# Optimization experiments

Hardware: AMD Instinct MI355X
Metric: run time of the kernel (lower is better)

The kernel has to match this reference:

```python
import jax, jax.numpy as jnp
import numpy as np

WS = 7       # window size
SHIFT = 3    # shift size (ws//2)
NH = 16      # num heads
DIM = 512    # channels
HH = 112
WW = 112
HIDDEN = int(DIM * 4.0)
EPS = 1e-5


def _rel_index():
    # Swin relative position index, [N, N] ints into the bias table
    coords = np.stack(np.meshgrid(np.arange(WS), np.arange(WS), indexing='ij')).reshape(2, -1)
    rel = coords[:, :, None] - coords[:, None, :]
    rel = rel.transpose(1, 2, 0) + (WS - 1)
    rel[:, :, 0] *= 2 * WS - 1
    return rel.sum(-1)


def _attn_mask():
    # shifted-window mask on HH x WW (already multiples of WS) -> [nW, N, N] with 0 / -1e9
    img = np.zeros((HH, WW), np.int32)
    cnt = 0
    sl = (slice(0, -WS), slice(-WS, -SHIFT), slice(-SHIFT, None))
    for h in sl:
        for w in sl:
            img[h, w] = cnt
            cnt += 1
    win = img.reshape(HH // WS, WS, WW // WS, WS).transpose(0, 2, 1, 3).reshape(-1, WS * WS)
    diff = win[:, None, :] - win[:, :, None]
    return np.where(diff == 0, 0.0, -1e9).astype(np.float32)


def setup_inputs() -> dict:
    key = jax.random.key(0)
    ks = jax.random.split(key, 8)
    s = 0.02
    return {
        'x': jax.random.normal(ks[0], (DIM, HH, WW), jnp.float32),
        'norm1_w': jnp.ones((DIM,), jnp.float32),
        'norm1_b': jnp.zeros((DIM,), jnp.float32),
        'qkv_w': jax.random.normal(ks[1], (3 * DIM, DIM), jnp.float32) * s,
        'qkv_b': jnp.zeros((3 * DIM,), jnp.float32),
        'proj_w': jax.random.normal(ks[2], (DIM, DIM), jnp.float32) * s,
        'proj_b': jnp.zeros((DIM,), jnp.float32),
        'rpb_table': jax.random.normal(ks[3], ((2 * WS - 1) ** 2, NH), jnp.float32) * s,
        'norm2_w': jnp.ones((DIM,), jnp.float32),
        'norm2_b': jnp.zeros((DIM,), jnp.float32),
        'fc1_w': jax.random.normal(ks[4], (HIDDEN, DIM), jnp.float32) * s,
        'fc1_b': jnp.zeros((HIDDEN,), jnp.float32),
        'fc2_w': jax.random.normal(ks[5], (DIM, HIDDEN), jnp.float32) * s,
        'fc2_b': jnp.zeros((DIM,), jnp.float32),
    }


def _ln(x_hwc, w, b):
    m = x_hwc.mean(-1, keepdims=True)
    v = x_hwc.var(-1, keepdims=True)
    return (x_hwc - m) / jnp.sqrt(v + EPS) * w + b


def reference(x, norm1_w, norm1_b, qkv_w, qkv_b, proj_w, proj_b, rpb_table,
              norm2_w, norm2_b, fc1_w, fc1_b, fc2_w, fc2_b):
    C, H, W = x.shape
    ws = WS
    N = ws * ws
    hd = C // NH
    scale = 1.0 / np.sqrt(hd).astype(np.float32)

    x_hwc = jnp.moveaxis(x, 0, -1)                       # [H,W,C]
    xn = _ln(x_hwc, norm1_w, norm1_b)
    xs = jnp.roll(xn, (-SHIFT, -SHIFT), (0, 1))          # cyclic shift
    # window partition -> [nW, N, C]
    xw = xs.reshape(H // ws, ws, W // ws, ws, C).transpose(0, 2, 1, 3, 4).reshape(-1, N, C)

    qkv = xw @ qkv_w.T + qkv_b                            # [nW,N,3C]
    q, k, v = jnp.split(qkv, 3, -1)
    heads = lambda t: t.reshape(-1, N, NH, hd).transpose(0, 2, 1, 3)  # [nW,H,N,hd]
    q, k, v = heads(q), heads(k), heads(v)

    attn = jnp.einsum('whnd,whmd->whnm', q * scale, k)    # [nW,H,N,N]
    idx = jnp.asarray(_rel_index().reshape(-1))
    bias = rpb_table[idx].reshape(N, N, NH).transpose(2, 0, 1)  # [H,N,N]
    mask = jnp.asarray(_attn_mask())                       # [nW,N,N]
    attn = attn + bias[None] + mask[:, None]
    attn = jax.nn.softmax(attn, -1)

    out = jnp.einsum('whnm,whmd->whnd', attn, v).transpose(0, 2, 1, 3).reshape(-1, N, C)
    out = out @ proj_w.T + proj_b
    # window unpartition + reverse shift
    out = out.reshape(H // ws, W // ws, ws, ws, C).transpose(0, 2, 1, 3, 4).reshape(H, W, C)
    out = jnp.roll(out, (SHIFT, SHIFT), (0, 1))

    x1 = x_hwc + out                                       # residual (DropPath rate 0)
    x2 = _ln(x1, norm2_w, norm2_b)
    h = jax.nn.gelu(x2.reshape(-1, C) @ fc1_w.T + fc1_b)
    m = (h @ fc2_w.T + fc2_b).reshape(H, W, C)
    y = x1 + m
    return jnp.moveaxis(y, -1, 0)                          # back to [C,H,W]
```

## Files before the change

### kernel.cpp

```cpp
#include <hip/hip_runtime.h>

#define NPIX 12544
#define CDIM 512
#define QKVN 1536
#define HIDDEN 2048

typedef unsigned short u16;
typedef unsigned int u32;

typedef short bf16x8 __attribute__((ext_vector_type(8)));
typedef float f32x4 __attribute__((ext_vector_type(4)));

static __device__ __forceinline__ u16 f2bf(float f) {
  u32 u = __float_as_uint(f);
  return (u16)((u + 0x7fffu + ((u >> 16) & 1u)) >> 16);
}
static __device__ __forceinline__ float bf2f(u32 bits16) {
  return __uint_as_float(bits16 << 16);
}
static __device__ __forceinline__ u32 pack2(float a, float b) {
  return (u32)f2bf(a) | ((u32)f2bf(b) << 16);
}
static __device__ __forceinline__ void unpack8(uint4 u, float* d) {
  d[0] = bf2f(u.x & 0xffffu); d[1] = bf2f(u.x >> 16);
  d[2] = bf2f(u.y & 0xffffu); d[3] = bf2f(u.y >> 16);
  d[4] = bf2f(u.z & 0xffffu); d[5] = bf2f(u.z >> 16);
  d[6] = bf2f(u.w & 0xffffu); d[7] = bf2f(u.w >> 16);
}
static __device__ __forceinline__ void async_ld16(const void* g, void* l) {
  __builtin_amdgcn_global_load_lds((__attribute__((address_space(1))) void*)g,
                                   (__attribute__((address_space(3))) void*)l, 16, 0, 0);
}

__global__ __launch_bounds__(256) void f32_to_bf16(const float* __restrict__ in, u16* __restrict__ out) {
  const int i = blockIdx.x * 256 + threadIdx.x;
  const float4 v = ((const float4*)in)[i];
  ushort4 u;
  u.x = f2bf(v.x); u.y = f2bf(v.y); u.z = f2bf(v.z); u.w = f2bf(v.w);
  ((ushort4*)out)[i] = u;
}

__global__ __launch_bounds__(256) void ln1_partial(const float* __restrict__ x,
                                                   float* __restrict__ psum, float* __restrict__ pssq) {
  const int p = blockIdx.x * 256 + threadIdx.x;
  const int c0 = blockIdx.y * 32;
  float s = 0.f, ss = 0.f;
#pragma unroll
  for (int c = 0; c < 32; c++) {
    const float v = x[(long)(c0 + c) * NPIX + p];
    s += v; ss += v * v;
  }
  psum[blockIdx.y * NPIX + p] = s;
  pssq[blockIdx.y * NPIX + p] = ss;
}

__global__ __launch_bounds__(256) void ln1_stats(const float* __restrict__ psum, const float* __restrict__ pssq,
                                                 float* __restrict__ mean, float* __restrict__ rstd) {
  const int p = blockIdx.x * 256 + threadIdx.x;
  float s = 0.f, ss = 0.f;
#pragma unroll
  for (int ch = 0; ch < 16; ch++) { s += psum[ch * NPIX + p]; ss += pssq[ch * NPIX + p]; }
  const float m = s * (1.f / 512.f);
  const float v = ss * (1.f / 512.f) - m * m;
  mean[p] = m;
  rstd[p] = rsqrtf(v + 1e-5f);
}

__global__ __launch_bounds__(256) void ln1_shift_part(const float* __restrict__ x,
    const float* __restrict__ mean, const float* __restrict__ rstd,
    const float* __restrict__ gw, const float* __restrict__ gb, u16* __restrict__ xw) {
  __shared__ float tile[32][65];
  const int p0 = blockIdx.x * 64;
  const int c0 = blockIdx.y * 32;
  const int t = threadIdx.x;
  {
    const int pl = t & 63;
    const int cl0 = t >> 6;
#pragma unroll
    for (int r = 0; r < 8; r++) {
      const int cl = r * 4 + cl0;
      tile[cl][pl] = x[(long)(c0 + cl) * NPIX + p0 + pl];
    }
  }
  __syncthreads();
  const int cl = t & 31;
  const int g = t >> 5;
  const float wc = gw[c0 + cl];
  const float bc = gb[c0 + cl];
#pragma unroll
  for (int pass = 0; pass < 8; pass++) {
    const int pl = pass * 8 + g;
    const int p = p0 + pl;
    const int h = p / 112;
    const int w = p - h * 112;
    int hs = h + 109; if (hs >= 112) hs -= 112;
    int ws2 = w + 109; if (ws2 >= 112) ws2 -= 112;
    const int hq = hs / 7, wq = ws2 / 7;
    const int tok = (hq * 16 + wq) * 49 + (hs - hq * 7) * 7 + (ws2 - wq * 7);
    const float val = (tile[cl][pl] - mean[p]) * rstd[p] * wc + bc;
    xw[(long)tok * 512 + c0 + cl] = f2bf(val);
  }
}

template<bool OUT_BF16, bool DO_GELU, bool REMAP>
__global__ __launch_bounds__(256, 2) void gemm_bt(
    const u16* __restrict__ A, const u16* __restrict__ B,
    const float* __restrict__ bias, void* __restrict__ out,
    const int N, const int K) {
  __shared__ __align__(16) u16 Asm[128 * 32];
  __shared__ __align__(16) u16 Bsm[128 * 32];
  const int M0 = blockIdx.x << 7;
  const int N0 = blockIdx.y << 7;
  const int t = threadIdx.x;
  const int wave = t >> 6;
  const int lane = t & 63;
  const int l15 = lane & 15;
  const int quad = lane >> 4;
  const int wm = wave & 1;
  const int wn = wave >> 1;

  f32x4 acc[4][4] = {};

  for (int k0 = 0; k0 < K; k0 += 32) {
#pragma unroll
    for (int i = 0; i < 2; i++) {
      const int flatbase = i * 256 + wave * 64;
      const int FL = flatbase + lane;
      const int row = FL >> 2;
      const int chunk = FL & 3;
      async_ld16(A + (long)(M0 + row) * K + k0 + chunk * 8, &Asm[flatbase * 8]);
      async_ld16(B + (long)(N0 + row) * K + k0 + chunk * 8, &Bsm[flatbase * 8]);
    }
    __syncthreads();
    bf16x8 af[4], bfr[4];
#pragma unroll
    for (int im = 0; im < 4; im++)
      af[im] = *(const bf16x8*)&Asm[(wm * 64 + im * 16 + l15) * 32 + quad * 8];
#pragma unroll
    for (int in = 0; in < 4; in++)
      bfr[in] = *(const bf16x8*)&Bsm[(wn * 64 + in * 16 + l15) * 32 + quad * 8];
#pragma unroll
    for (int im = 0; im < 4; im++)
#pragma unroll
      for (int in = 0; in < 4; in++)
        acc[im][in] = __builtin_amdgcn_mfma_f32_16x16x32_bf16(af[im], bfr[in], acc[im][in], 0, 0, 0);
    __syncthreads();
  }

#pragma unroll
  for (int im = 0; im < 4; im++) {
#pragma unroll
    for (int in = 0; in < 4; in++) {
      const int col = N0 + wn * 64 + in * 16 + l15;
      const float bv = bias[col];
#pragma unroll
      for (int r = 0; r < 4; r++) {
        const int row = M0 + wm * 64 + im * 16 + quad * 4 + r;
        float v = acc[im][in][r] + bv;
        if (DO_GELU) {
          const float z2 = 1.5957691216f * (v + 0.044715f * v * v * v);
          v = v / (1.0f + __expf(-z2));
        }
        long orow = row;
        if (REMAP) {
          const int win = row / 49;
          const int nn = row - win * 49;
          const int nq = nn / 7;
          const int hs = (win >> 4) * 7 + nq;
          const int wsx = (win & 15) * 7 + (nn - nq * 7);
          int h = hs + 3; if (h >= 112) h -= 112;
          int w = wsx + 3; if (w >= 112) w -= 112;
          orow = h * 112 + w;
        }
        if (OUT_BF16) ((u16*)out)[orow * (long)N + col] = f2bf(v);
        else          ((float*)out)[orow * (long)N + col] = v;
      }
    }
  }
}

__global__ __launch_bounds__(64) void attn_kernel(
    const u16* __restrict__ qkv, const float* __restrict__ rpb, u16* __restrict__ out) {
  const int win = blockIdx.x >> 4;
  const int head = blockIdx.x & 15;
  __shared__ __align__(16) float ks[49][32];
  __shared__ __align__(16) float vs[49][32];
  __shared__ float bias_s[169];
  __shared__ int label_s[49];
  const int l = threadIdx.x;
  for (int idx = l; idx < 169; idx += 64) bias_s[idx] = rpb[idx * 16 + head];
  float q[32];
  if (l < 49) {
    const long base = (long)(win * 49 + l) * 1536 + head * 32;
    const uint4* qp = (const uint4*)(qkv + base);
    const uint4* kp = (const uint4*)(qkv + base + 512);
    const uint4* vp = (const uint4*)(qkv + base + 1024);
#pragma unroll
    for (int cc = 0; cc < 4; cc++) {
      unpack8(qp[cc], &q[cc * 8]);
      unpack8(kp[cc], &ks[l][cc * 8]);
      unpack8(vp[cc], &vs[l][cc * 8]);
    }
    const int ri = l / 7, ci = l - (l / 7) * 7;
    const int hs = (win >> 4) * 7 + ri;
    const int wsx = (win & 15) * 7 + ci;
    label_s[l] = (hs < 105 ? 0 : (hs < 109 ? 1 : 2)) * 3 + (wsx < 105 ? 0 : (wsx < 109 ? 1 : 2));
  }
  __syncthreads();
  if (l >= 49) return;
  const int ri = l / 7, ci = l - (l / 7) * 7;
  const int mylab = label_s[l];
  float sr[49];
  float mx = -1e30f;
#pragma unroll
  for (int j = 0; j < 49; j++) {
    const float4* kj = (const float4*)ks[j];
    float s = 0.f;
#pragma unroll
    for (int c = 0; c < 8; c++) {
      const float4 kv = kj[c];
      s += q[c * 4 + 0] * kv.x + q[c * 4 + 1] * kv.y + q[c * 4 + 2] * kv.z + q[c * 4 + 3] * kv.w;
    }
    const int rj = j / 7, cj = j - (j / 7) * 7;
    float sv = s * 0.17677669529663687f + bias_s[(ri - rj + 6) * 13 + (ci - cj + 6)];
    if (mylab != label_s[j]) sv -= 1e9f;
    sr[j] = sv;
    mx = fmaxf(mx, sv);
  }
  float sum = 0.f;
#pragma unroll
  for (int j = 0; j < 49; j++) { const float e = __expf(sr[j] - mx); sr[j] = e; sum += e; }
  float o[32];
#pragma unroll
  for (int d = 0; d < 32; d++) o[d] = 0.f;
#pragma unroll
  for (int j = 0; j < 49; j++) {
    const float pj = sr[j];
    const float4* vj = (const float4*)vs[j];
#pragma unroll
    for (int c = 0; c < 8; c++) {
      const float4 vv = vj[c];
      o[c * 4 + 0] += pj * vv.x; o[c * 4 + 1] += pj * vv.y;
      o[c * 4 + 2] += pj * vv.z; o[c * 4 + 3] += pj * vv.w;
    }
  }
  const float inv = 1.f / sum;
  uint4* outp = (uint4*)(out + (long)(win * 49 + l) * 512 + head * 32);
#pragma unroll
  for (int cc = 0; cc < 4; cc++) {
    uint4 u;
    u.x = pack2(o[cc * 8 + 0] * inv, o[cc * 8 + 1] * inv);
    u.y = pack2(o[cc * 8 + 2] * inv, o[cc * 8 + 3] * inv);
    u.z = pack2(o[cc * 8 + 4] * inv, o[cc * 8 + 5] * inv);
    u.w = pack2(o[cc * 8 + 6] * inv, o[cc * 8 + 7] * inv);
    outp[cc] = u;
  }
}

__global__ __launch_bounds__(256) void resid_kernel(const float* __restrict__ x,
    const float* __restrict__ proj, float* __restrict__ x1) {
  __shared__ float tile[32][65];
  const int p0 = blockIdx.x * 64;
  const int c0 = blockIdx.y * 32;
  const int t = threadIdx.x;
  {
    const int pl = t & 63;
    const int cl0 = t >> 6;
#pragma unroll
    for (int r = 0; r < 8; r++) {
      const int cl = r * 4 + cl0;
      tile[cl][pl] = x[(long)(c0 + cl) * NPIX + p0 + pl];
    }
  }
  __syncthreads();
  const int cl = t & 31;
  const int g = t >> 5;
#pragma unroll
  for (int pass = 0; pass < 8; pass++) {
    const int pl = pass * 8 + g;
    const long idx = (long)(p0 + pl) * 512 + c0 + cl;
    x1[idx] = tile[cl][pl] + proj[idx];
  }
}

__global__ __launch_bounds__(256) void ln2_apply(const float* __restrict__ x1,
    const float* __restrict__ gw, const float* __restrict__ gb, u16* __restrict__ x2) {
  const int wave = threadIdx.x >> 6;
  const int lane = threadIdx.x & 63;
  const int p = blockIdx.x * 4 + wave;
  const float4* row = (const float4*)(x1 + (long)p * 512);
  const float4 a = row[lane * 2];
  const float4 b = row[lane * 2 + 1];
  float s = a.x + a.y + a.z + a.w + b.x + b.y + b.z + b.w;
  float ss = a.x * a.x + a.y * a.y + a.z * a.z + a.w * a.w
           + b.x * b.x + b.y * b.y + b.z * b.z + b.w * b.w;
#pragma unroll
  for (int o = 32; o > 0; o >>= 1) { s += __shfl_xor(s, o); ss += __shfl_xor(ss, o); }
  const float m = s * (1.f / 512.f);
  const float var = ss * (1.f / 512.f) - m * m;
  const float rs = rsqrtf(var + 1e-5f);
  const float4 w0 = ((const float4*)gw)[lane * 2];
  const float4 w1 = ((const float4*)gw)[lane * 2 + 1];
  const float4 b0 = ((const float4*)gb)[lane * 2];
  const float4 b1 = ((const float4*)gb)[lane * 2 + 1];
  uint4 u;
  u.x = pack2((a.x - m) * rs * w0.x + b0.x, (a.y - m) * rs * w0.y + b0.y);
  u.y = pack2((a.z - m) * rs * w0.z + b0.z, (a.w - m) * rs * w0.w + b0.w);
  u.z = pack2((b.x - m) * rs * w1.x + b1.x, (b.y - m) * rs * w1.y + b1.y);
  u.w = pack2((b.z - m) * rs * w1.z + b1.z, (b.w - m) * rs * w1.w + b1.w);
  ((uint4*)(x2 + (long)p * 512))[lane] = u;
}

__global__ __launch_bounds__(256) void final_kernel(const float* __restrict__ x1,
    const float* __restrict__ mm, float* __restrict__ y) {
  __shared__ float tile[32][65];
  const int p0 = blockIdx.x * 64;
  const int c0 = blockIdx.y * 32;
  const int t = threadIdx.x;
  {
    const int cl = t & 31;
    const int g = t >> 5;
#pragma unroll
    for (int pass = 0; pass < 8; pass++) {
      const int pl = pass * 8 + g;
      const long idx = (long)(p0 + pl) * 512 + c0 + cl;
      tile[cl][pl] = x1[idx] + mm[idx];
    }
  }
  __syncthreads();
  const int pl = t & 63;
  const int cl0 = t >> 6;
#pragma unroll
  for (int r = 0; r < 8; r++) {
    const int cl = r * 4 + cl0;
    y[(long)(c0 + cl) * NPIX + p0 + pl] = tile[cl][pl];
  }
}

extern "C" void kernel_launch(void* const* d_in, const int* in_sizes, int n_in,
                              void* d_out, int out_size, void* d_ws, size_t ws_size,
                              hipStream_t stream) {
  (void)in_sizes; (void)n_in; (void)out_size; (void)ws_size;
  const float* x      = (const float*)d_in[0];
  const float* n1w    = (const float*)d_in[1];
  const float* n1b    = (const float*)d_in[2];
  const float* qkv_w  = (const float*)d_in[3];
  const float* qkv_b  = (const float*)d_in[4];
  const float* proj_w = (const float*)d_in[5];
  const float* proj_b = (const float*)d_in[6];
  const float* rpb    = (const float*)d_in[7];
  const float* n2w    = (const float*)d_in[8];
  const float* n2b    = (const float*)d_in[9];
  const float* fc1_w  = (const float*)d_in[10];
  const float* fc1_b  = (const float*)d_in[11];
  const float* fc2_w  = (const float*)d_in[12];
  const float* fc2_b  = (const float*)d_in[13];
  float* y = (float*)d_out;

  char* base = (char*)d_ws;
  size_t off = 0;
  auto alloc = [&](size_t b) { char* p = base + off; off += (b + 255) & ~(size_t)255; return p; };
  float* mean1 = (float*)alloc((size_t)NPIX * 4);
  float* rstd1 = (float*)alloc((size_t)NPIX * 4);
  float* psum  = (float*)alloc((size_t)16 * NPIX * 4);
  float* pssq  = (float*)alloc((size_t)16 * NPIX * 4);
  u16* Wq = (u16*)alloc((size_t)QKVN * CDIM * 2);
  u16* Wp = (u16*)alloc((size_t)CDIM * CDIM * 2);
  u16* W1 = (u16*)alloc((size_t)HIDDEN * CDIM * 2);
  u16* W2 = (u16*)alloc((size_t)CDIM * HIDDEN * 2);
  u16* bufA = (u16*)alloc((size_t)NPIX * CDIM * 2);
  char* bufB = alloc((size_t)NPIX * QKVN * 2);
  float* x1 = (float*)alloc((size_t)NPIX * CDIM * 4);
  u16* hbuf = (u16*)alloc((size_t)NPIX * HIDDEN * 2);

  u16* xw      = bufA;
  u16* qkvbuf  = (u16*)bufB;
  u16* attnout = bufA;
  float* projout = (float*)bufB;
  u16* x2 = bufA;
  float* mbuf = (float*)bufB;

  f32_to_bf16<<<QKVN * CDIM / 1024, 256, 0, stream>>>(qkv_w, Wq);
  f32_to_bf16<<<CDIM * CDIM / 1024, 256, 0, stream>>>(proj_w, Wp);
  f32_to_bf16<<<HIDDEN * CDIM / 1024, 256, 0, stream>>>(fc1_w, W1);
  f32_to_bf16<<<CDIM * HIDDEN / 1024, 256, 0, stream>>>(fc2_w, W2);

  ln1_partial<<<dim3(49, 16), 256, 0, stream>>>(x, psum, pssq);
  ln1_stats<<<49, 256, 0, stream>>>(psum, pssq, mean1, rstd1);
  ln1_shift_part<<<dim3(196, 16), 256, 0, stream>>>(x, mean1, rstd1, n1w, n1b, xw);

  gemm_bt<true, false, false><<<dim3(98, QKVN / 128), 256, 0, stream>>>(xw, Wq, qkv_b, qkvbuf, QKVN, CDIM);
  attn_kernel<<<256 * 16, 64, 0, stream>>>(qkvbuf, rpb, attnout);
  gemm_bt<false, false, true><<<dim3(98, CDIM / 128), 256, 0, stream>>>(attnout, Wp, proj_b, projout, CDIM, CDIM);

  resid_kernel<<<dim3(196, 16), 256, 0, stream>>>(x, projout, x1);
  ln2_apply<<<NPIX / 4, 256, 0, stream>>>(x1, n2w, n2b, x2);

  gemm_bt<true, true, false><<<dim3(98, HIDDEN / 128), 256, 0, stream>>>(x2, W1, fc1_b, hbuf, HIDDEN, CDIM);
  gemm_bt<false, false, false><<<dim3(98, CDIM / 128), 256, 0, stream>>>(hbuf, W2, fc2_b, mbuf, CDIM, HIDDEN);

  final_kernel<<<dim3(196, 16), 256, 0, stream>>>(x1, mbuf, y);
}
```

Measured before the change: 382.0 us.

## Rewrite window attention with bf16 MFMA and a precomputed bias-mask table

Replaces the scalar per-thread window attention (one 64-thread block per window-head, with fp32 dot products in registers) with an MFMA kernel. Each wave handles one head of a window, with QK^T and PV done via 16x16x32 bf16 MFMA, swizzled LDS layouts for V-transpose and P, and softmax reductions done with cross-lane shuffles. A new prepass builds a padded 64x64 bias-plus-mask table per (window class, head), so the attention kernel does a single load per score instead of index math and label comparisons. The change also rounds P and the outputs by bf16 truncation rather than round-to-nearest, which adds some precision risk.

```diff
diff --git a/kernel.cpp b/kernel.cpp
--- a/kernel.cpp
+++ b/kernel.cpp
@@ -15,17 +15,11 @@
   u32 u = __float_as_uint(f);
   return (u16)((u + 0x7fffu + ((u >> 16) & 1u)) >> 16);
 }
-static __device__ __forceinline__ float bf2f(u32 bits16) {
-  return __uint_as_float(bits16 << 16);
-}
 static __device__ __forceinline__ u32 pack2(float a, float b) {
   return (u32)f2bf(a) | ((u32)f2bf(b) << 16);
 }
-static __device__ __forceinline__ void unpack8(uint4 u, float* d) {
-  d[0] = bf2f(u.x & 0xffffu); d[1] = bf2f(u.x >> 16);
-  d[2] = bf2f(u.y & 0xffffu); d[3] = bf2f(u.y >> 16);
-  d[4] = bf2f(u.z & 0xffffu); d[5] = bf2f(u.z >> 16);
-  d[6] = bf2f(u.w & 0xffffu); d[7] = bf2f(u.w >> 16);
+static __device__ __forceinline__ u32 packtrunc2(float lo, float hi) {
+  return __builtin_amdgcn_perm(__float_as_uint(hi), __float_as_uint(lo), 0x07060302u);
 }
 static __device__ __forceinline__ void async_ld16(const void* g, void* l) {
   __builtin_amdgcn_global_load_lds((__attribute__((address_space(1))) void*)g,
@@ -179,81 +173,164 @@
   }
 }
 
-__global__ __launch_bounds__(64) void attn_kernel(
-    const u16* __restrict__ qkv, const float* __restrict__ rpb, u16* __restrict__ out) {
-  const int win = blockIdx.x >> 4;
+__global__ __launch_bounds__(256) void build_biasT(const float* __restrict__ rpb, float* __restrict__ biasT) {
+  const int cls = blockIdx.x >> 4;
   const int head = blockIdx.x & 15;
-  __shared__ __align__(16) float ks[49][32];
-  __shared__ __align__(16) float vs[49][32];
-  __shared__ float bias_s[169];
-  __shared__ int label_s[49];
-  const int l = threadIdx.x;
-  for (int idx = l; idx < 169; idx += 64) bias_s[idx] = rpb[idx * 16 + head];
-  float q[32];
-  if (l < 49) {
-    const long base = (long)(win * 49 + l) * 1536 + head * 32;
-    const uint4* qp = (const uint4*)(qkv + base);
-    const uint4* kp = (const uint4*)(qkv + base + 512);
-    const uint4* vp = (const uint4*)(qkv + base + 1024);
-#pragma unroll
-    for (int cc = 0; cc < 4; cc++) {
-      unpack8(qp[cc], &q[cc * 8]);
-      unpack8(kp[cc], &ks[l][cc * 8]);
-      unpack8(vp[cc], &vs[l][cc * 8]);
-    }
-    const int ri = l / 7, ci = l - (l / 7) * 7;
-    const int hs = (win >> 4) * 7 + ri;
-    const int wsx = (win & 15) * 7 + ci;
-    label_s[l] = (hs < 105 ? 0 : (hs < 109 ? 1 : 2)) * 3 + (wsx < 105 ? 0 : (wsx < 109 ? 1 : 2));
+  for (int e = threadIdx.x; e < 4096; e += 256) {
+    const int j = e >> 6;
+    const int i = e & 63;
+    float v;
+    if (j >= 49) v = -1e9f;
+    else if (i >= 49) v = 0.f;
+    else {
+      const int ri = i / 7, ci = i - (i / 7) * 7;
+      const int rj = j / 7, cj = j - (j / 7) * 7;
+      v = rpb[((ri - rj + 6) * 13 + (ci - cj + 6)) * 16 + head];
+      const int lhi = (cls & 2) ? (ri < 4 ? 1 : 2) : 0;
+      const int lwi = (cls & 1) ? (ci < 4 ? 1 : 2) : 0;
+      const int lhj = (cls & 2) ? (rj < 4 ? 1 : 2) : 0;
+      const int lwj = (cls & 1) ? (cj < 4 ? 1 : 2) : 0;
+      if (lhi * 3 + lwi != lhj * 3 + lwj) v = -1e9f;
+    }
+    biasT[(long)blockIdx.x * 4096 + e] = v;
+  }
+}
+
+__global__ __launch_bounds__(256, 3) void attn_mfma(
+    const u16* __restrict__ qkv, const float* __restrict__ biasT, u16* __restrict__ out) {
+  __shared__ __align__(16) u16 slds[24576];
+  const int t = threadIdx.x;
+  const int wave = t >> 6;
+  const int lane = t & 63;
+  const int l15 = lane & 15;
+  const int quad = lane >> 4;
+  const int win = blockIdx.x >> 2;
+  const int head = (blockIdx.x & 3) * 4 + wave;
+  const int cls = (((win >> 4) == 15) ? 2 : 0) | (((win & 15) == 15) ? 1 : 0);
+
+  u16* Qb  = slds + wave * 6144;
+  u16* Kb  = Qb + 2048;
+  u16* Vtb = Qb + 4096;
+  u16* Pb  = Qb;
+
+  const int rrow = lane >> 2;
+  const int chunk = lane & 3;
+  uint4 vv[4];
+#pragma unroll
+  for (int it = 0; it < 4; it++) {
+    const int row = it * 16 + rrow;
+    const int jc = row < 49 ? row : 48;
+    const long gbase = (long)(win * 49 + jc) * 1536 + head * 32 + chunk * 8;
+    async_ld16(qkv + gbase,       Qb + it * 512 + lane * 8);
+    async_ld16(qkv + gbase + 512, Kb + it * 512 + lane * 8);
+    vv[it] = *(const uint4*)(qkv + gbase + 1024);
   }
   __syncthreads();
-  if (l >= 49) return;
-  const int ri = l / 7, ci = l - (l / 7) * 7;
-  const int mylab = label_s[l];
-  float sr[49];
-  float mx = -1e30f;
-#pragma unroll
-  for (int j = 0; j < 49; j++) {
-    const float4* kj = (const float4*)ks[j];
+
+#pragma unroll
+  for (int it = 0; it < 4; it++) {
+    const int row = it * 16 + rrow;
+    const u32* w = (const u32*)&vv[it];
+#pragma unroll
+    for (int tt = 0; tt < 8; tt++) {
+      const int d = chunk * 8 + tt;
+      const u16 val = (tt & 1) ? (u16)(w[tt >> 1] >> 16) : (u16)(w[tt >> 1] & 0xffffu);
+      Vtb[d * 64 + (row ^ (((d >> 2) & 3) << 4))] = val;
+    }
+  }
+
+  bf16x8 kfrag[4], qfrag[4];
+#pragma unroll
+  for (int jm = 0; jm < 4; jm++)
+    kfrag[jm] = *(const bf16x8*)(Kb + (jm * 16 + l15) * 32 + quad * 8);
+#pragma unroll
+  for (int in = 0; in < 4; in++)
+    qfrag[in] = *(const bf16x8*)(Qb + (in * 16 + l15) * 32 + quad * 8);
+  f32x4 sacc[4][4] = {};
+#pragma unroll
+  for (int jm = 0; jm < 4; jm++)
+#pragma unroll
+    for (int in = 0; in < 4; in++)
+      sacc[jm][in] = __builtin_amdgcn_mfma_f32_16x16x32_bf16(kfrag[jm], qfrag[in], sacc[jm][in], 0, 0, 0);
+
+  const float* bT = biasT + (long)(cls * 16 + head) * 4096;
+  const float sc = 0.17677669529663687f;
+#pragma unroll
+  for (int jm = 0; jm < 4; jm++) {
+    const float* bp = bT + (jm * 16 + quad * 4) * 64 + l15;
+#pragma unroll
+    for (int in = 0; in < 4; in++)
+#pragma unroll
+      for (int r = 0; r < 4; r++)
+        sacc[jm][in][r] = sacc[jm][in][r] * sc + bp[r * 64 + in * 16];
+  }
+  float linv[4];
+#pragma unroll
+  for (int in = 0; in < 4; in++) {
+    float m = -1e30f;
+#pragma unroll
+    for (int jm = 0; jm < 4; jm++)
+#pragma unroll
+      for (int r = 0; r < 4; r++) m = fmaxf(m, sacc[jm][in][r]);
+    m = fmaxf(m, __shfl_xor(m, 16));
+    m = fmaxf(m, __shfl_xor(m, 32));
     float s = 0.f;
 #pragma unroll
-    for (int c = 0; c < 8; c++) {
-      const float4 kv = kj[c];
-      s += q[c * 4 + 0] * kv.x + q[c * 4 + 1] * kv.y + q[c * 4 + 2] * kv.z + q[c * 4 + 3] * kv.w;
-    }
-    const int rj = j / 7, cj = j - (j / 7) * 7;
-    float sv = s * 0.17677669529663687f + bias_s[(ri - rj + 6) * 13 + (ci - cj + 6)];
-    if (mylab != label_s[j]) sv -= 1e9f;
-    sr[j] = sv;
-    mx = fmaxf(mx, sv);
-  }
-  float sum = 0.f;
-#pragma unroll
-  for (int j = 0; j < 49; j++) { const float e = __expf(sr[j] - mx); sr[j] = e; sum += e; }
-  float o[32];
-#pragma unroll
-  for (int d = 0; d < 32; d++) o[d] = 0.f;
-#pragma unroll
-  for (int j = 0; j < 49; j++) {
-    const float pj = sr[j];
-    const float4* vj = (const float4*)vs[j];
-#pragma unroll
-    for (int c = 0; c < 8; c++) {
-      const float4 vv = vj[c];
-      o[c * 4 + 0] += pj * vv.x; o[c * 4 + 1] += pj * vv.y;
-      o[c * 4 + 2] += pj * vv.z; o[c * 4 + 3] += pj * vv.w;
-    }
-  }
-  const float inv = 1.f / sum;
-  uint4* outp = (uint4*)(out + (long)(win * 49 + l) * 512 + head * 32);
-#pragma unroll
-  for (int cc = 0; cc < 4; cc++) {
-    uint4 u;
-    u.x = pack2(o[cc * 8 + 0] * inv, o[cc * 8 + 1] * inv);
-    u.y = pack2(o[cc * 8 + 2] * inv, o[cc * 8 + 3] * inv);
-    u.z = pack2(o[cc * 8 + 4] * inv, o[cc * 8 + 5] * inv);
-    u.w = pack2(o[cc * 8 + 6] * inv, o[cc * 8 + 7] * inv);
-    outp[cc] = u;
+    for (int jm = 0; jm < 4; jm++)
+#pragma unroll
+      for (int r = 0; r < 4; r++) {
+        const float e = __expf(sacc[jm][in][r] - m);
+        sacc[jm][in][r] = e; s += e;
+      }
+    s += __shfl_xor(s, 16);
+    s += __shfl_xor(s, 32);
+    linv[in] = __builtin_amdgcn_rcpf(s);
+  }
+
+#pragma unroll
+  for (int in = 0; in < 4; in++) {
+    const int i = in * 16 + l15;
+    const int rot = (l15 & 3) << 4;
+#pragma unroll
+    for (int jm = 0; jm < 4; jm++) {
+      const u32 lo = packtrunc2(sacc[jm][in][0], sacc[jm][in][1]);
+      const u32 hi = packtrunc2(sacc[jm][in][2], sacc[jm][in][3]);
+      uint2 u; u.x = lo; u.y = hi;
+      *(uint2*)(Pb + i * 64 + ((jm * 16 + quad * 4) ^ rot)) = u;
+    }
+  }
+
+  f32x4 oacc[2][4] = {};
+#pragma unroll
+  for (int ks = 0; ks < 2; ks++) {
+    bf16x8 vtf[2], pf[4];
+#pragma unroll
+    for (int dm = 0; dm < 2; dm++)
+      vtf[dm] = *(const bf16x8*)(Vtb + (dm * 16 + l15) * 64 + ((ks * 32 + quad * 8) ^ ((l15 >> 2) << 4)));
+#pragma unroll
+    for (int in = 0; in < 4; in++)
+      pf[in] = *(const bf16x8*)(Pb + (in * 16 + l15) * 64 + ((ks * 32 + quad * 8) ^ ((l15 & 3) << 4)));
+#pragma unroll
+    for (int dm = 0; dm < 2; dm++)
+#pragma unroll
+      for (int in = 0; in < 4; in++)
+        oacc[dm][in] = __builtin_amdgcn_mfma_f32_16x16x32_bf16(vtf[dm], pf[in], oacc[dm][in], 0, 0, 0);
+  }
+
+#pragma unroll
+  for (int in = 0; in < 4; in++) {
+    const int i = in * 16 + l15;
+    if (i < 49) {
+      const float inv = linv[in];
+      const long base = (long)(win * 49 + i) * 512 + head * 32 + quad * 4;
+#pragma unroll
+      for (int dm = 0; dm < 2; dm++) {
+        const float v0 = oacc[dm][in][0] * inv, v1 = oacc[dm][in][1] * inv;
+        const float v2 = oacc[dm][in][2] * inv, v3 = oacc[dm][in][3] * inv;
+        uint2 u; u.x = packtrunc2(v0, v1); u.y = packtrunc2(v2, v3);
+        *(uint2*)(out + base + dm * 16) = u;
+      }
+    }
   }
 }
 
@@ -368,6 +445,7 @@
   u16* Wp = (u16*)alloc((size_t)CDIM * CDIM * 2);
   u16* W1 = (u16*)alloc((size_t)HIDDEN * CDIM * 2);
   u16* W2 = (u16*)alloc((size_t)CDIM * HIDDEN * 2);
+  float* biasT = (float*)alloc((size_t)4 * 16 * 4096 * 4);
   u16* bufA = (u16*)alloc((size_t)NPIX * CDIM * 2);
   char* bufB = alloc((size_t)NPIX * QKVN * 2);
   float* x1 = (float*)alloc((size_t)NPIX * CDIM * 4);
@@ -384,13 +462,14 @@
   f32_to_bf16<<<CDIM * CDIM / 1024, 256, 0, stream>>>(proj_w, Wp);
   f32_to_bf16<<<HIDDEN * CDIM / 1024, 256, 0, stream>>>(fc1_w, W1);
   f32_to_bf16<<<CDIM * HIDDEN / 1024, 256, 0, stream>>>(fc2_w, W2);
+  build_biasT<<<64, 256, 0, stream>>>(rpb, biasT);
 
   ln1_partial<<<dim3(49, 16), 256, 0, stream>>>(x, psum, pssq);
   ln1_stats<<<49, 256, 0, stream>>>(psum, pssq, mean1, rstd1);
   ln1_shift_part<<<dim3(196, 16), 256, 0, stream>>>(x, mean1, rstd1, n1w, n1b, xw);
 
   gemm_bt<true, false, false><<<dim3(98, QKVN / 128), 256, 0, stream>>>(xw, Wq, qkv_b, qkvbuf, QKVN, CDIM);
-  attn_kernel<<<256 * 16, 64, 0, stream>>>(qkvbuf, rpb, attnout);
+  attn_mfma<<<1024, 256, 0, stream>>>(qkvbuf, biasT, attnout);
   gemm_bt<false, false, true><<<dim3(98, CDIM / 128), 256, 0, stream>>>(attnout, Wp, proj_b, projout, CDIM, CDIM);
 
   resid_kernel<<<dim3(196, 16), 256, 0, stream>>>(x, projout, x1);
```

Result: faster. 329.2 us (-13.8%).
